# Kernel tuning notes

Hardware: AMD Instinct MI355X
Metric: run time of the kernel (lower is better)

Reference implementation:

```python
import jax, jax.numpy as jnp
import numpy as np

N_NODES = 50000
N_EDGES = 800000
N_GRAPHS = 50
N_OBS = 4
N_FEAT = 64
N_LAYERS = 3


def setup_inputs() -> dict:
    key = jax.random.key(0)
    ks = jax.random.split(key, 12)
    x = jax.random.normal(ks[0], (N_NODES, N_OBS), dtype=jnp.float32)
    # every node appears at least once as a target (col) so degree > 0 everywhere
    row = jax.random.randint(ks[1], (N_EDGES,), 0, N_NODES, dtype=jnp.int32)
    col = jnp.concatenate([
        jnp.arange(N_NODES, dtype=jnp.int32),
        jax.random.randint(ks[2], (N_EDGES - N_NODES,), 0, N_NODES, dtype=jnp.int32),
    ])
    edge_index = jnp.stack([row, col])  # [2, E]
    batch = jnp.repeat(jnp.arange(N_GRAPHS, dtype=jnp.int32), N_NODES // N_GRAPHS)

    def w(k, shape):
        fan_in = shape[0]
        return jax.random.normal(k, shape, dtype=jnp.float32) / jnp.sqrt(jnp.float32(fan_in))

    return {
        "x": x,
        "W_init": w(ks[3], (N_OBS, N_FEAT)),
        "W_e1": w(ks[4], (N_OBS, N_FEAT - 1)),
        "W_e2": w(ks[5], (N_FEAT, N_FEAT)),
        "W_msg": w(ks[6], (N_LAYERS, 2 * N_FEAT, N_FEAT)),
        "W_upd": w(ks[7], (N_LAYERS, 2 * N_FEAT, N_FEAT)),
        "W_pool": w(ks[8], (N_FEAT, N_FEAT)),
        "W_read": w(ks[9], (2 * N_FEAT, 1)),
        "b_read": jnp.zeros((1,), dtype=jnp.float32),
        "edge_index": edge_index,
        "batch": batch,
        "batch_size": N_GRAPHS,
    }


def reference(x, W_init, W_e1, W_e2, W_msg, W_upd, W_pool, W_read, b_read,
              edge_index, batch, batch_size):
    n = x.shape[0]
    row, col = edge_index[0], edge_index[1]
    # in-degree at target nodes (PyG degree(col, N))
    deg = jax.ops.segment_sum(jnp.ones_like(col, dtype=x.dtype), col, num_segments=n)
    deg_inv = (1.0 / deg)[:, None]  # [N,1]

    # node init embedding
    cur = jax.nn.relu(x @ W_init)  # [N,F]

    # EdgeAndNodeEmbeddingLayer
    h = jax.nn.relu(x @ W_e1)  # [N,F-1]
    agg = deg_inv * jax.ops.segment_sum(h[row], col, num_segments=n)  # [N,F-1]
    y = jnp.concatenate([agg, (deg / deg.max())[:, None]], axis=1)  # [N,F]
    edge_emb = jax.nn.relu(y @ W_e2)  # [N,F]

    # UpdateNodeEmbeddingLayer x n_layers
    for i in range(W_msg.shape[0]):
        nagg = deg_inv * jax.ops.segment_sum(cur[row], col, num_segments=n)
        msg = jax.nn.relu(jnp.concatenate([nagg, edge_emb], axis=-1) @ W_msg[i])
        cur = jax.nn.relu(jnp.concatenate([cur, msg], axis=-1) @ W_upd[i])

    # ReadoutLayer (graphs are equal-sized, batch is sorted -> means[batch])
    counts = jax.ops.segment_sum(jnp.ones((n,), dtype=x.dtype), batch, num_segments=batch_size)
    means = jax.ops.segment_sum(cur, batch, num_segments=batch_size) / counts[:, None]
    global_pool = means[batch]  # [N,F]
    f_pooled = global_pool @ W_pool
    features = jax.nn.relu(jnp.concatenate([f_pooled, cur], axis=-1))  # [N,2F]
    out = features @ W_read + b_read  # [N,1]
    return out
```

## Files before the change

### kernel.cpp

```cpp
#include <hip/hip_runtime.h>
#include <hip/hip_bf16.h>

#define N_NODES 50000
#define N_EDGES 800000
#define NF      64
#define NG      50
#define NPG     (N_NODES / NG)
#define SCAN_NBLK ((N_NODES + 255) / 256)
#define MCHUNK  20
#define MROWS   (NPG / MCHUNK)
#define NTILES  (N_NODES / 16)
#define GATHER_BLKS ((NTILES + 3) / 4)
#define FP_CHUNKS 896
#define FP_CHSZ  ((N_EDGES + FP_CHUNKS - 1) / FP_CHUNKS)
#define FP_NPP   (N_NODES / 8)
#define DEG_BLKS (FP_CHUNKS * 8)
#define INIT_BLKS ((N_NODES * 32 + 255) / 256)
#define DEGS 5

typedef __attribute__((ext_vector_type(8))) short bf16x8;
typedef __attribute__((ext_vector_type(4))) float f32x4;
typedef unsigned short u16;
typedef unsigned char u8;

__device__ inline unsigned pkbf(float a, float b) {
    unsigned ua = __float_as_uint(a) + 0x8000u;
    unsigned ub = __float_as_uint(b) + 0x8000u;
    return (ua >> 16) | (ub & 0xFFFF0000u);
}
__device__ inline short bf1(float a) {
    return (short)((__float_as_uint(a) + 0x8000u) >> 16);
}
__device__ inline float lo2f(unsigned u) { return __uint_as_float(u << 16); }
__device__ inline float hi2f(unsigned u) { return __uint_as_float(u & 0xFFFF0000u); }
__device__ inline void accp(float2* a, uint4 v) {
    a[0].x += lo2f(v.x); a[0].y += hi2f(v.x);
    a[1].x += lo2f(v.y); a[1].y += hi2f(v.y);
    a[2].x += lo2f(v.z); a[2].y += hi2f(v.z);
    a[3].x += lo2f(v.w); a[3].y += hi2f(v.w);
}

__global__ void k_deg_init(const int* __restrict__ col, int* __restrict__ deg,
                           u8* __restrict__ epos,
                           const float* __restrict__ x, const float* __restrict__ Wi,
                           const float* __restrict__ We1,
                           u16* __restrict__ cur, u16* __restrict__ h) {
    if (blockIdx.x < DEG_BLKS) {
        int part = blockIdx.x & 7, chunk = blockIdx.x >> 3;
        int lo = part * FP_NPP, hi = lo + FP_NPP;
        int e0 = chunk * FP_CHSZ;
        int e1 = min(N_EDGES, e0 + FP_CHSZ);
        for (int e = e0 + threadIdx.x; e < e1; e += 256) {
            int c = col[e];
            if (c >= lo && c < hi) {
                int pos = atomicAdd(&deg[c << DEGS], 1);
                epos[e] = (u8)pos;
            }
        }
        return;
    }
    int idx = (blockIdx.x - DEG_BLKS) * 256 + threadIdx.x;
    int node = idx >> 5, q = idx & 31;
    if (node >= N_NODES) return;
    int f0 = 2 * q, f1 = 2 * q + 1;
    float4 xv = ((const float4*)x)[node];
    float c0 = xv.x * Wi[f0] + xv.y * Wi[64 + f0] + xv.z * Wi[128 + f0] + xv.w * Wi[192 + f0];
    float c1 = xv.x * Wi[f1] + xv.y * Wi[64 + f1] + xv.z * Wi[128 + f1] + xv.w * Wi[192 + f1];
    ((unsigned*)cur)[node * 32 + q] = pkbf(fmaxf(c0, 0.f), fmaxf(c1, 0.f));
    float h0 = xv.x * We1[f0] + xv.y * We1[63 + f0] + xv.z * We1[126 + f0] + xv.w * We1[189 + f0];
    h0 = fmaxf(h0, 0.f);
    float h1 = 0.f;
    if (f1 < 63) {
        h1 = xv.x * We1[f1] + xv.y * We1[63 + f1] + xv.z * We1[126 + f1] + xv.w * We1[189 + f1];
        h1 = fmaxf(h1, 0.f);
    }
    ((unsigned*)h)[node * 32 + q] = pkbf(h0, h1);
}

__global__ void k_blocksum(const int* __restrict__ deg, int* __restrict__ partials,
                           int* __restrict__ dmax, int* __restrict__ hist) {
    __shared__ int lh[256];
    int t = threadIdx.x;
    lh[t] = 0;
    __syncthreads();
    int i = blockIdx.x * 256 + t;
    int d = (i < N_NODES) ? deg[i << DEGS] : 0;
    if (i < N_NODES) atomicAdd(&lh[min(d, 255)], 1);
    int v = d, m = d;
    for (int off = 32; off; off >>= 1) {
        v += __shfl_xor(v, off, 64);
        m = max(m, __shfl_xor(m, off, 64));
    }
    __shared__ int s[4];
    if ((t & 63) == 0) { s[t >> 6] = v; atomicMax(dmax, m); }
    __syncthreads();
    if (t == 0) partials[blockIdx.x] = s[0] + s[1] + s[2] + s[3];
    if (lh[t]) atomicAdd(&hist[t], lh[t]);
}

__global__ __launch_bounds__(256) void k_scanfinal2(
        const int* __restrict__ deg, const int* __restrict__ partials,
        const int* __restrict__ hist, int* __restrict__ rowptr,
        int* __restrict__ binBump, int* __restrict__ perm) {
    int b = blockIdx.x, t = threadIdx.x;
    __shared__ int lh[256], lbase[256];
    lh[t] = 0;
    int p = (t < b) ? partials[t] : 0;
    for (int off = 32; off; off >>= 1) p += __shfl_xor(p, off, 64);
    __shared__ int sr[4];
    if ((t & 63) == 0) sr[t >> 6] = p;
    __syncthreads();
    int prev = sr[0] + sr[1] + sr[2] + sr[3];
    int i = b * 256 + t;
    int v = (i < N_NODES) ? deg[i << DEGS] : 0;
    int bin = min(v, 255);
    int rank = 0;
    if (i < N_NODES) rank = atomicAdd(&lh[bin], 1);
    __shared__ int s[256];
    int hv = hist[t];
    s[t] = hv;
    __syncthreads();
    for (int off = 1; off < 256; off <<= 1) {
        int u = (t >= off) ? s[t - off] : 0;
        __syncthreads();
        s[t] += u;
        __syncthreads();
    }
    int total = s[255];
    int hpref = total - s[t];
    __syncthreads();
    s[t] = v;
    __syncthreads();
    for (int off = 1; off < 256; off <<= 1) {
        int u = (t >= off) ? s[t - off] : 0;
        __syncthreads();
        s[t] += u;
        __syncthreads();
    }
    int ex = prev + s[t] - v;
    if (i < N_NODES) rowptr[i] = ex;
    if (b == 0 && t == 0) rowptr[N_NODES] = N_EDGES;
    __syncthreads();
    if (lh[t] > 0) lbase[t] = hpref + atomicAdd(&binBump[t], lh[t]);
    __syncthreads();
    if (i < N_NODES) perm[lbase[bin] + rank] = i;
}

__global__ void k_fill(const int* __restrict__ row, const int* __restrict__ col,
                       const int* __restrict__ rowptr, const u8* __restrict__ epos,
                       u16* __restrict__ csr) {
    int part = blockIdx.x & 7, chunk = blockIdx.x >> 3;
    int lo = part * FP_NPP, hi = lo + FP_NPP;
    int e0 = chunk * FP_CHSZ;
    int e1 = min(N_EDGES, e0 + FP_CHSZ);
    for (int e = e0 + threadIdx.x; e < e1; e += 256) {
        int c = col[e];
        if (c >= lo && c < hi)
            csr[rowptr[c] + epos[e]] = (u16)row[e];
    }
}

__device__ inline void gather_tile(const u16* __restrict__ src,
                                   const int* __restrict__ rowptr,
                                   const u16* __restrict__ csr,
                                   int node, int m, int q, int wv,
                                   short (*AT)[16][64]) {
    int beg = rowptr[node], end = rowptr[node + 1];
    float2 ac[8];
#pragma unroll
    for (int i = 0; i < 8; i++) ac[i] = make_float2(0.f, 0.f);
    int j = beg;
    for (; j + 5 < end; j += 6) {
        int r0 = csr[j],     r1 = csr[j + 1], r2 = csr[j + 2];
        int r3 = csr[j + 3], r4 = csr[j + 4], r5 = csr[j + 5];
        const uint4* p0 = (const uint4*)(src + (size_t)r0 * 64 + q * 16);
        const uint4* p1 = (const uint4*)(src + (size_t)r1 * 64 + q * 16);
        const uint4* p2 = (const uint4*)(src + (size_t)r2 * 64 + q * 16);
        const uint4* p3 = (const uint4*)(src + (size_t)r3 * 64 + q * 16);
        const uint4* p4 = (const uint4*)(src + (size_t)r4 * 64 + q * 16);
        const uint4* p5 = (const uint4*)(src + (size_t)r5 * 64 + q * 16);
        uint4 v00 = p0[0], v01 = p0[1];
        uint4 v10 = p1[0], v11 = p1[1];
        uint4 v20 = p2[0], v21 = p2[1];
        uint4 v30 = p3[0], v31 = p3[1];
        uint4 v40 = p4[0], v41 = p4[1];
        uint4 v50 = p5[0], v51 = p5[1];
        accp(ac, v00); accp(ac + 4, v01);
        accp(ac, v10); accp(ac + 4, v11);
        accp(ac, v20); accp(ac + 4, v21);
        accp(ac, v30); accp(ac + 4, v31);
        accp(ac, v40); accp(ac + 4, v41);
        accp(ac, v50); accp(ac + 4, v51);
    }
    for (; j + 3 < end; j += 4) {
        int r0 = csr[j], r1 = csr[j + 1], r2 = csr[j + 2], r3 = csr[j + 3];
        const uint4* p0 = (const uint4*)(src + (size_t)r0 * 64 + q * 16);
        const uint4* p1 = (const uint4*)(src + (size_t)r1 * 64 + q * 16);
        const uint4* p2 = (const uint4*)(src + (size_t)r2 * 64 + q * 16);
        const uint4* p3 = (const uint4*)(src + (size_t)r3 * 64 + q * 16);
        uint4 v00 = p0[0], v01 = p0[1];
        uint4 v10 = p1[0], v11 = p1[1];
        uint4 v20 = p2[0], v21 = p2[1];
        uint4 v30 = p3[0], v31 = p3[1];
        accp(ac, v00); accp(ac + 4, v01);
        accp(ac, v10); accp(ac + 4, v11);
        accp(ac, v20); accp(ac + 4, v21);
        accp(ac, v30); accp(ac + 4, v31);
    }
    for (; j < end; j++) {
        int r = csr[j];
        const uint4* p = (const uint4*)(src + (size_t)r * 64 + q * 16);
        uint4 v0 = p[0], v1 = p[1];
        accp(ac, v0); accp(ac + 4, v1);
    }
    float inv = 1.0f / (float)(end - beg);
    uint4 lo, hi;
    lo.x = pkbf(ac[0].x * inv, ac[0].y * inv);
    lo.y = pkbf(ac[1].x * inv, ac[1].y * inv);
    lo.z = pkbf(ac[2].x * inv, ac[2].y * inv);
    lo.w = pkbf(ac[3].x * inv, ac[3].y * inv);
    hi.x = pkbf(ac[4].x * inv, ac[4].y * inv);
    hi.y = pkbf(ac[5].x * inv, ac[5].y * inv);
    hi.z = pkbf(ac[6].x * inv, ac[6].y * inv);
    hi.w = pkbf(ac[7].x * inv, ac[7].y * inv);
    *(uint4*)&AT[wv][m][((2 * q) ^ (m & 7)) * 8]     = lo;
    *(uint4*)&AT[wv][m][((2 * q + 1) ^ (m & 7)) * 8] = hi;
}

__global__ __launch_bounds__(256) void k_edge_f(
        const u16* __restrict__ h, const int* __restrict__ rowptr,
        const u16* __restrict__ csr, const int* __restrict__ dmax,
        const float* __restrict__ We2, const int* __restrict__ perm,
        u16* __restrict__ ee) {
    __shared__ unsigned SB[2][4][64][4];
    __shared__ short AT[4][16][64];
    int t = threadIdx.x;
    for (int F = t; F < 512; F += 256) {
        int ks = F >> 8, tile = (F >> 6) & 3, ln = F & 63;
        int c = ln & 15, qq = ln >> 4;
        const float* W = We2 + (ks * 32 + qq * 8) * 64 + tile * 16 + c;
        unsigned d0 = pkbf(W[0],       W[64]);
        unsigned d1 = pkbf(W[2 * 64],  W[3 * 64]);
        unsigned d2 = pkbf(W[4 * 64],  W[5 * 64]);
        unsigned d3 = pkbf(W[6 * 64],  W[7 * 64]);
        int slot = ln ^ ((ln >> 3) & 7);
        SB[ks][tile][slot][0] = d0; SB[ks][tile][slot][1] = d1;
        SB[ks][tile][slot][2] = d2; SB[ks][tile][slot][3] = d3;
    }
    __syncthreads();
    int wv = t >> 6, lane = t & 63;
    int m = lane & 15, quad = lane >> 4;
    int slot = lane ^ ((lane >> 3) & 7);
    float idm = 1.0f / (float)dmax[0];
    for (int tb = blockIdx.x * 4 + wv; tb < NTILES; tb += gridDim.x * 4) {
        int base = tb * 16;
        int pn = perm[base + m];
        gather_tile(h, rowptr, csr, pn, m, quad, wv, AT);
        float dv = (float)(rowptr[pn + 1] - rowptr[pn]) * idm;
        int prw[4];
#pragma unroll
        for (int r = 0; r < 4; r++) prw[r] = perm[base + quad * 4 + r];
        f32x4 acc[4];
#pragma unroll
        for (int i = 0; i < 4; i++) acc[i] = (f32x4){0.f, 0.f, 0.f, 0.f};
#pragma unroll
        for (int ks = 0; ks < 2; ks++) {
            int gp = (ks * 4 + quad) ^ (m & 7);
            bf16x8 a = *(const bf16x8*)&AT[wv][m][gp * 8];
            if (ks == 1 && quad == 3) a[7] = bf1(dv);
#pragma unroll
            for (int tile = 0; tile < 4; tile++) {
                bf16x8 b = *(const bf16x8*)&SB[ks][tile][slot][0];
                acc[tile] = __builtin_amdgcn_mfma_f32_16x16x32_bf16(a, b, acc[tile], 0, 0, 0);
            }
        }
#pragma unroll
        for (int tile = 0; tile < 4; tile++)
#pragma unroll
            for (int r = 0; r < 4; r++)
                ee[(size_t)prw[r] * 64 + tile * 16 + m] =
                    (u16)bf1(fmaxf(acc[tile][r], 0.f));
    }
}

template <bool F32OUT>
__global__ __launch_bounds__(256) void k_flayer(
        const u16* __restrict__ cur, const u16* __restrict__ ee,
        const int* __restrict__ rowptr, const u16* __restrict__ csr,
        const float* __restrict__ Wm, const float* __restrict__ Wu,
        const int* __restrict__ perm, void* __restrict__ outp) {
    __shared__ unsigned SB[2][4][4][64][4];
    __shared__ short XT[4][16][64];
    int t = threadIdx.x;
    for (int F = t; F < 2048; F += 256) {
        int g = F >> 10, ks = (F >> 8) & 3, tile = (F >> 6) & 3, ln = F & 63;
        int c = ln & 15, qq = ln >> 4;
        const float* W = (g ? Wu : Wm) + (ks * 32 + qq * 8) * 64 + tile * 16 + c;
        unsigned d0 = pkbf(W[0],      W[64]);
        unsigned d1 = pkbf(W[2 * 64], W[3 * 64]);
        unsigned d2 = pkbf(W[4 * 64], W[5 * 64]);
        unsigned d3 = pkbf(W[6 * 64], W[7 * 64]);
        int slot = ln ^ ((ln >> 3) & 7);
        SB[g][ks][tile][slot][0] = d0; SB[g][ks][tile][slot][1] = d1;
        SB[g][ks][tile][slot][2] = d2; SB[g][ks][tile][slot][3] = d3;
    }
    __syncthreads();
    int wv = t >> 6, lane = t & 63;
    int m = lane & 15, quad = lane >> 4;
    int slot = lane ^ ((lane >> 3) & 7);
    for (int tb = blockIdx.x * 4 + wv; tb < NTILES; tb += gridDim.x * 4) {
        int base = tb * 16;
        int pn = perm[base + m];
        gather_tile(cur, rowptr, csr, pn, m, quad, wv, XT);
        const u16* erow = ee  + (size_t)pn * 64;
        const u16* crow = cur + (size_t)pn * 64;
        int prw[4];
#pragma unroll
        for (int r = 0; r < 4; r++) prw[r] = perm[base + quad * 4 + r];
        f32x4 acc[4];
#pragma unroll
        for (int i = 0; i < 4; i++) acc[i] = (f32x4){0.f, 0.f, 0.f, 0.f};
#pragma unroll
        for (int ks = 0; ks < 4; ks++) {
            bf16x8 a;
            if (ks < 2) {
                int gp = (ks * 4 + quad) ^ (m & 7);
                a = *(const bf16x8*)&XT[wv][m][gp * 8];
            } else {
                a = *(const bf16x8*)(erow + (ks - 2) * 32 + quad * 8);
            }
#pragma unroll
            for (int tile = 0; tile < 4; tile++) {
                bf16x8 b = *(const bf16x8*)&SB[0][ks][tile][slot][0];
                acc[tile] = __builtin_amdgcn_mfma_f32_16x16x32_bf16(a, b, acc[tile], 0, 0, 0);
            }
        }
#pragma unroll
        for (int tile = 0; tile < 4; tile++)
#pragma unroll
            for (int r = 0; r < 4; r++) {
                int node = quad * 4 + r;
                int f = tile * 16 + m;
                int sidx = (((f >> 3) ^ (node & 7)) << 3) | (f & 7);
                XT[wv][node][sidx] = bf1(fmaxf(acc[tile][r], 0.f));
            }
#pragma unroll
        for (int i = 0; i < 4; i++) acc[i] = (f32x4){0.f, 0.f, 0.f, 0.f};
#pragma unroll
        for (int ks = 0; ks < 4; ks++) {
            bf16x8 a;
            if (ks < 2) {
                a = *(const bf16x8*)(crow + ks * 32 + quad * 8);
            } else {
                int gp = ((ks - 2) * 4 + quad) ^ (m & 7);
                a = *(const bf16x8*)&XT[wv][m][gp << 3];
            }
#pragma unroll
            for (int tile = 0; tile < 4; tile++) {
                bf16x8 b = *(const bf16x8*)&SB[1][ks][tile][slot][0];
                acc[tile] = __builtin_amdgcn_mfma_f32_16x16x32_bf16(a, b, acc[tile], 0, 0, 0);
            }
        }
#pragma unroll
        for (int tile = 0; tile < 4; tile++)
#pragma unroll
            for (int r = 0; r < 4; r++) {
                float v = fmaxf(acc[tile][r], 0.f);
                size_t oi = (size_t)prw[r] * 64 + tile * 16 + m;
                if (F32OUT) ((float*)outp)[oi] = v;
                else        ((u16*)outp)[oi] = (u16)bf1(v);
            }
    }
}

__global__ __launch_bounds__(256) void k_means2(const float* __restrict__ cur,
                                                float* __restrict__ pmeans) {
    int g = blockIdx.x / MCHUNK;
    int c = blockIdx.x % MCHUNK;
    int t = threadIdx.x, f = t & 63, q = t >> 6;
    int base = g * NPG + c * MROWS;
    float acc = 0.f;
    for (int n = base + q; n < base + MROWS; n += 4) acc += cur[(size_t)n * 64 + f];
    __shared__ float red[4][64];
    red[q][f] = acc;
    __syncthreads();
    if (q == 0)
        pmeans[(size_t)(g * MCHUNK + c) * 64 + f] =
            red[0][f] + red[1][f] + red[2][f] + red[3][f];
}

__global__ __launch_bounds__(256) void k_pool2(
        const float* __restrict__ pmeans, const float* __restrict__ Wp,
        const float* __restrict__ Wr, float* __restrict__ r1) {
    __shared__ float sm[4][64];
    int wv = threadIdx.x >> 6, lane = threadIdx.x & 63;
    for (int g = wv; g < NG; g += 4) {
        float m = 0.f;
        const float* pm = pmeans + (size_t)g * MCHUNK * 64 + lane;
#pragma unroll
        for (int c = 0; c < MCHUNK; c++) m += pm[c * 64];
        sm[wv][lane] = m * (1.0f / NPG);
        float a2 = 0.f;
#pragma unroll 16
        for (int k = 0; k < 64; k++) a2 = fmaf(sm[wv][k], Wp[k * 64 + lane], a2);
        float v = fmaxf(a2, 0.f) * Wr[lane];
        for (int off = 32; off; off >>= 1) v += __shfl_xor(v, off, 64);
        if (lane == 0) r1[g] = v;
    }
}

__global__ void k_read2(const float* __restrict__ cur, const float* __restrict__ r1,
                        const int* __restrict__ batch, const float* __restrict__ Wr,
                        const float* __restrict__ br, float* __restrict__ out) {
    int idx = blockIdx.x * 256 + threadIdx.x;
    int node = idx >> 4;
    if (node >= N_NODES) return;
    int q = idx & 15;
    float4 c = *(const float4*)(cur + (size_t)node * 64 + q * 4);
    float4 w = *(const float4*)(Wr + 64 + q * 4);
    float v = fmaxf(c.x, 0.f) * w.x + fmaxf(c.y, 0.f) * w.y
            + fmaxf(c.z, 0.f) * w.z + fmaxf(c.w, 0.f) * w.w;
    v += __shfl_xor(v, 1, 64); v += __shfl_xor(v, 2, 64);
    v += __shfl_xor(v, 4, 64); v += __shfl_xor(v, 8, 64);
    if (q == 0) out[node] = v + r1[batch[node]] + br[0];
}

extern "C" void kernel_launch(void* const* d_in, const int* in_sizes, int n_in,
                              void* d_out, int out_size, void* d_ws, size_t ws_size,
                              hipStream_t stream) {
    const float* x    = (const float*)d_in[0];
    const float* Wi   = (const float*)d_in[1];
    const float* We1  = (const float*)d_in[2];
    const float* We2  = (const float*)d_in[3];
    const float* Wm   = (const float*)d_in[4];
    const float* Wu   = (const float*)d_in[5];
    const float* Wp   = (const float*)d_in[6];
    const float* Wr   = (const float*)d_in[7];
    const float* br   = (const float*)d_in[8];
    const int*   ei   = (const int*)d_in[9];
    const int*   batch= (const int*)d_in[10];
    const int* row = ei;
    const int* col = ei + N_EDGES;
    float* out = (float*)d_out;

    char* w = (char*)d_ws;
    size_t off = 0;
    auto carve = [&](size_t bytes) -> void* {
        void* p = (void*)(w + off);
        off += (bytes + 255) & ~(size_t)255;
        return p;
    };
    int*   deg      = (int*)carve((size_t)N_NODES * 4 * 32);
    int*   dmax     = (int*)carve(256);
    int*   hist     = (int*)carve(256 * 4);
    int*   binBump  = (int*)carve(256 * 4);
    size_t zero_span = off;
    int*   rowptr   = (int*)carve((size_t)(N_NODES + 1) * 4);
    u8*    epos     = (u8*)carve((size_t)N_EDGES);
    u16*   csr      = (u16*)carve((size_t)N_EDGES * 2);
    int*   partials = (int*)carve((size_t)SCAN_NBLK * 4);
    int*   perm     = (int*)carve((size_t)N_NODES * 4);
    float* pmeans   = (float*)carve((size_t)NG * MCHUNK * 64 * 4);
    u16*   bufA     = (u16*)carve((size_t)N_NODES * 64 * 2);
    u16*   bufB     = (u16*)carve((size_t)N_NODES * 64 * 2);
    u16*   ee       = (u16*)carve((size_t)N_NODES * 64 * 2);
    float* curF     = (float*)carve((size_t)N_NODES * 64 * 4);
    float* r1       = (float*)carve((size_t)NG * 4);

    hipMemsetAsync(d_ws, 0, zero_span, stream);

    k_deg_init<<<DEG_BLKS + INIT_BLKS, 256, 0, stream>>>(col, deg, epos,
                                                         x, Wi, We1, bufA, bufB);
    k_blocksum  <<<SCAN_NBLK, 256, 0, stream>>>(deg, partials, dmax, hist);
    k_scanfinal2<<<SCAN_NBLK, 256, 0, stream>>>(deg, partials, hist, rowptr,
                                                binBump, perm);
    k_fill      <<<DEG_BLKS, 256, 0, stream>>>(row, col, rowptr, epos, csr);

    k_edge_f<<<GATHER_BLKS, 256, 0, stream>>>(bufB, rowptr, csr, dmax, We2, perm, ee);

    k_flayer<false><<<GATHER_BLKS, 256, 0, stream>>>(bufA, ee, rowptr, csr,
                                                     Wm, Wu, perm, bufB);
    k_flayer<false><<<GATHER_BLKS, 256, 0, stream>>>(bufB, ee, rowptr, csr,
                                                     Wm + 128 * 64, Wu + 128 * 64,
                                                     perm, bufA);
    k_flayer<true> <<<GATHER_BLKS, 256, 0, stream>>>(bufA, ee, rowptr, csr,
                                                     Wm + 2 * 128 * 64, Wu + 2 * 128 * 64,
                                                     perm, curF);

    k_means2<<<NG * MCHUNK, 256, 0, stream>>>(curF, pmeans);
    k_pool2 <<<1, 256, 0, stream>>>(pmeans, Wp, Wr, r1);
    k_read2<<<(N_NODES * 16 + 255) / 256, 256, 0, stream>>>(curF, r1, batch, Wr, br, out);
}
```

Baseline: 296.9 us.

## Build CSR via two-pass bucket sort instead of atomic degree count plus fill

Replaces the global-atomic degree counting (with padded counters) and separate fill pass with a two-pass bucket sort. Edges are first scattered into 256-node buckets using shared-memory histograms, then each bucket is locally sorted into CSR, which also yields degrees and rowptr. This cuts global atomics and the repeated column scans done by eight partition blocks, at the cost of a fixed-capacity bucket buffer (6144 per bucket) that overflows if a bucket receives more edges than expected.

```diff
diff --git a/kernel.cpp b/kernel.cpp
--- a/kernel.cpp
+++ b/kernel.cpp
@@ -11,12 +11,11 @@
 #define MROWS   (NPG / MCHUNK)
 #define NTILES  (N_NODES / 16)
 #define GATHER_BLKS ((NTILES + 3) / 4)
-#define FP_CHUNKS 896
-#define FP_CHSZ  ((N_EDGES + FP_CHUNKS - 1) / FP_CHUNKS)
-#define FP_NPP   (N_NODES / 8)
-#define DEG_BLKS (FP_CHUNKS * 8)
 #define INIT_BLKS ((N_NODES * 32 + 255) / 256)
-#define DEGS 5
+#define NBKT ((N_NODES + 255) / 256)
+#define BKT_CAP 6144
+#define P1_EPB 4096
+#define P1_BLKS ((N_EDGES + P1_EPB - 1) / P1_EPB)
 
 typedef __attribute__((ext_vector_type(8))) short bf16x8;
 typedef __attribute__((ext_vector_type(4))) float f32x4;
@@ -40,26 +39,41 @@
     a[3].x += lo2f(v.w); a[3].y += hi2f(v.w);
 }
 
-__global__ void k_deg_init(const int* __restrict__ col, int* __restrict__ deg,
-                           u8* __restrict__ epos,
-                           const float* __restrict__ x, const float* __restrict__ Wi,
-                           const float* __restrict__ We1,
-                           u16* __restrict__ cur, u16* __restrict__ h) {
-    if (blockIdx.x < DEG_BLKS) {
-        int part = blockIdx.x & 7, chunk = blockIdx.x >> 3;
-        int lo = part * FP_NPP, hi = lo + FP_NPP;
-        int e0 = chunk * FP_CHSZ;
-        int e1 = min(N_EDGES, e0 + FP_CHSZ);
-        for (int e = e0 + threadIdx.x; e < e1; e += 256) {
-            int c = col[e];
-            if (c >= lo && c < hi) {
-                int pos = atomicAdd(&deg[c << DEGS], 1);
-                epos[e] = (u8)pos;
+__global__ void k_bucket_init(const int* __restrict__ row, const int* __restrict__ col,
+                              int* __restrict__ bktCnt, unsigned* __restrict__ bktData,
+                              const float* __restrict__ x, const float* __restrict__ Wi,
+                              const float* __restrict__ We1,
+                              u16* __restrict__ cur, u16* __restrict__ h) {
+    if (blockIdx.x < P1_BLKS) {
+        __shared__ int lh[256], lbase[256];
+        int t = threadIdx.x;
+        lh[t] = 0;
+        __syncthreads();
+        int e0 = blockIdx.x * P1_EPB;
+        int myb[16], myr[16];
+        unsigned mypk[16];
+#pragma unroll
+        for (int i = 0; i < 16; i++) {
+            int e = e0 + i * 256 + t;
+            myb[i] = -1;
+            if (e < N_EDGES) {
+                int c = col[e];
+                mypk[i] = ((unsigned)c << 16) | (unsigned)row[e];
+                int b = c >> 8;
+                myb[i] = b;
+                myr[i] = atomicAdd(&lh[b], 1);
             }
         }
+        __syncthreads();
+        if (lh[t] > 0) lbase[t] = atomicAdd(&bktCnt[t], lh[t]);
+        __syncthreads();
+#pragma unroll
+        for (int i = 0; i < 16; i++)
+            if (myb[i] >= 0)
+                bktData[(size_t)myb[i] * BKT_CAP + lbase[myb[i]] + myr[i]] = mypk[i];
         return;
     }
-    int idx = (blockIdx.x - DEG_BLKS) * 256 + threadIdx.x;
+    int idx = (blockIdx.x - P1_BLKS) * 256 + threadIdx.x;
     int node = idx >> 5, q = idx & 31;
     if (node >= N_NODES) return;
     int f0 = 2 * q, f1 = 2 * q + 1;
@@ -77,42 +91,74 @@
     ((unsigned*)h)[node * 32 + q] = pkbf(h0, h1);
 }
 
-__global__ void k_blocksum(const int* __restrict__ deg, int* __restrict__ partials,
+__global__ __launch_bounds__(256) void k_bsort(
+        const unsigned* __restrict__ bktData, const int* __restrict__ bktCnt,
+        int* __restrict__ deg, int* __restrict__ rowptr, u16* __restrict__ csr) {
+    int b = blockIdx.x, t = threadIdx.x;
+    int cnt = bktCnt[b];
+    int p = (t < b) ? bktCnt[t] : 0;
+    for (int off = 32; off; off >>= 1) p += __shfl_xor(p, off, 64);
+    __shared__ int sr[4];
+    if ((t & 63) == 0) sr[t >> 6] = p;
+    __shared__ int lh[256];
+    lh[t] = 0;
+    __syncthreads();
+    int prev = sr[0] + sr[1] + sr[2] + sr[3];
+    const unsigned* bd = bktData + (size_t)b * BKT_CAP;
+    for (int i = t; i < cnt; i += 256)
+        atomicAdd(&lh[(bd[i] >> 16) & 255], 1);
+    __syncthreads();
+    int myh = lh[t];
+    __shared__ int s[256];
+    s[t] = myh;
+    __syncthreads();
+    for (int off = 1; off < 256; off <<= 1) {
+        int u = (t >= off) ? s[t - off] : 0;
+        __syncthreads();
+        s[t] += u;
+        __syncthreads();
+    }
+    __shared__ int lof[256];
+    lof[t] = s[t] - myh;
+    int node = b * 256 + t;
+    if (node < N_NODES) { deg[node] = myh; rowptr[node] = prev + lof[t]; }
+    if (b == 0 && t == 0) rowptr[N_NODES] = N_EDGES;
+    __shared__ int cur[256];
+    cur[t] = 0;
+    __syncthreads();
+    for (int i = t; i < cnt; i += 256) {
+        unsigned pk = bd[i];
+        int ln = (pk >> 16) & 255;
+        int pos = atomicAdd(&cur[ln], 1);
+        csr[prev + lof[ln] + pos] = (u16)(pk & 0xFFFFu);
+    }
+}
+
+__global__ void k_blocksum(const int* __restrict__ deg,
                            int* __restrict__ dmax, int* __restrict__ hist) {
     __shared__ int lh[256];
     int t = threadIdx.x;
     lh[t] = 0;
     __syncthreads();
     int i = blockIdx.x * 256 + t;
-    int d = (i < N_NODES) ? deg[i << DEGS] : 0;
+    int d = (i < N_NODES) ? deg[i] : 0;
     if (i < N_NODES) atomicAdd(&lh[min(d, 255)], 1);
-    int v = d, m = d;
-    for (int off = 32; off; off >>= 1) {
-        v += __shfl_xor(v, off, 64);
-        m = max(m, __shfl_xor(m, off, 64));
-    }
-    __shared__ int s[4];
-    if ((t & 63) == 0) { s[t >> 6] = v; atomicMax(dmax, m); }
-    __syncthreads();
-    if (t == 0) partials[blockIdx.x] = s[0] + s[1] + s[2] + s[3];
+    int m = d;
+    for (int off = 32; off; off >>= 1) m = max(m, __shfl_xor(m, off, 64));
+    if ((t & 63) == 0) atomicMax(dmax, m);
+    __syncthreads();
     if (lh[t]) atomicAdd(&hist[t], lh[t]);
 }
 
-__global__ __launch_bounds__(256) void k_scanfinal2(
-        const int* __restrict__ deg, const int* __restrict__ partials,
-        const int* __restrict__ hist, int* __restrict__ rowptr,
+__global__ __launch_bounds__(256) void k_permsort(
+        const int* __restrict__ deg, const int* __restrict__ hist,
         int* __restrict__ binBump, int* __restrict__ perm) {
     int b = blockIdx.x, t = threadIdx.x;
     __shared__ int lh[256], lbase[256];
     lh[t] = 0;
-    int p = (t < b) ? partials[t] : 0;
-    for (int off = 32; off; off >>= 1) p += __shfl_xor(p, off, 64);
-    __shared__ int sr[4];
-    if ((t & 63) == 0) sr[t >> 6] = p;
-    __syncthreads();
-    int prev = sr[0] + sr[1] + sr[2] + sr[3];
+    __syncthreads();
     int i = b * 256 + t;
-    int v = (i < N_NODES) ? deg[i << DEGS] : 0;
+    int v = (i < N_NODES) ? deg[i] : 0;
     int bin = min(v, 255);
     int rank = 0;
     if (i < N_NODES) rank = atomicAdd(&lh[bin], 1);
@@ -128,36 +174,9 @@
     }
     int total = s[255];
     int hpref = total - s[t];
-    __syncthreads();
-    s[t] = v;
-    __syncthreads();
-    for (int off = 1; off < 256; off <<= 1) {
-        int u = (t >= off) ? s[t - off] : 0;
-        __syncthreads();
-        s[t] += u;
-        __syncthreads();
-    }
-    int ex = prev + s[t] - v;
-    if (i < N_NODES) rowptr[i] = ex;
-    if (b == 0 && t == 0) rowptr[N_NODES] = N_EDGES;
-    __syncthreads();
     if (lh[t] > 0) lbase[t] = hpref + atomicAdd(&binBump[t], lh[t]);
     __syncthreads();
     if (i < N_NODES) perm[lbase[bin] + rank] = i;
-}
-
-__global__ void k_fill(const int* __restrict__ row, const int* __restrict__ col,
-                       const int* __restrict__ rowptr, const u8* __restrict__ epos,
-                       u16* __restrict__ csr) {
-    int part = blockIdx.x & 7, chunk = blockIdx.x >> 3;
-    int lo = part * FP_NPP, hi = lo + FP_NPP;
-    int e0 = chunk * FP_CHSZ;
-    int e1 = min(N_EDGES, e0 + FP_CHSZ);
-    for (int e = e0 + threadIdx.x; e < e1; e += 256) {
-        int c = col[e];
-        if (c >= lo && c < hi)
-            csr[rowptr[c] + epos[e]] = (u16)row[e];
-    }
 }
 
 __device__ inline void gather_tile(const u16* __restrict__ src,
@@ -450,15 +469,15 @@
         off += (bytes + 255) & ~(size_t)255;
         return p;
     };
-    int*   deg      = (int*)carve((size_t)N_NODES * 4 * 32);
     int*   dmax     = (int*)carve(256);
     int*   hist     = (int*)carve(256 * 4);
     int*   binBump  = (int*)carve(256 * 4);
+    int*   bktCnt   = (int*)carve(256 * 4);
     size_t zero_span = off;
+    unsigned* bktData = (unsigned*)carve((size_t)NBKT * BKT_CAP * 4);
+    int*   deg      = (int*)carve((size_t)N_NODES * 4);
     int*   rowptr   = (int*)carve((size_t)(N_NODES + 1) * 4);
-    u8*    epos     = (u8*)carve((size_t)N_EDGES);
     u16*   csr      = (u16*)carve((size_t)N_EDGES * 2);
-    int*   partials = (int*)carve((size_t)SCAN_NBLK * 4);
     int*   perm     = (int*)carve((size_t)N_NODES * 4);
     float* pmeans   = (float*)carve((size_t)NG * MCHUNK * 64 * 4);
     u16*   bufA     = (u16*)carve((size_t)N_NODES * 64 * 2);
@@ -469,12 +488,11 @@
 
     hipMemsetAsync(d_ws, 0, zero_span, stream);
 
-    k_deg_init<<<DEG_BLKS + INIT_BLKS, 256, 0, stream>>>(col, deg, epos,
-                                                         x, Wi, We1, bufA, bufB);
-    k_blocksum  <<<SCAN_NBLK, 256, 0, stream>>>(deg, partials, dmax, hist);
-    k_scanfinal2<<<SCAN_NBLK, 256, 0, stream>>>(deg, partials, hist, rowptr,
-                                                binBump, perm);
-    k_fill      <<<DEG_BLKS, 256, 0, stream>>>(row, col, rowptr, epos, csr);
+    k_bucket_init<<<P1_BLKS + INIT_BLKS, 256, 0, stream>>>(row, col, bktCnt, bktData,
+                                                           x, Wi, We1, bufA, bufB);
+    k_bsort   <<<NBKT, 256, 0, stream>>>(bktData, bktCnt, deg, rowptr, csr);
+    k_blocksum<<<SCAN_NBLK, 256, 0, stream>>>(deg, dmax, hist);
+    k_permsort<<<SCAN_NBLK, 256, 0, stream>>>(deg, hist, binBump, perm);
 
     k_edge_f<<<GATHER_BLKS, 256, 0, stream>>>(bufB, rowptr, csr, dmax, We2, perm, ee);
 
```

Result: faster. 262.1 us (-11.7%).
